# Kernel tuning notes

Measured on AMD Instinct MI355X. Metric: run time of the kernel, lower is better.

The kernel has to match this reference:

```python
import jax, jax.numpy as jnp
import numpy as np

N, F_IN, F_OUT = 8192, 512, 256


def setup_inputs() -> dict:
    key = jax.random.key(0)
    k1, k2, k3, k4 = jax.random.split(key, 4)
    x = jax.random.normal(k1, (N, F_IN), dtype=jnp.float32)
    adj = jax.random.randint(k2, (N, N), 0, 2, dtype=jnp.int32)
    # xavier_uniform with gain=1.414
    limW = 1.414 * np.sqrt(6.0 / (F_IN + F_OUT))
    W = jax.random.uniform(k3, (F_IN, F_OUT), dtype=jnp.float32, minval=-limW, maxval=limW)
    lima = 1.414 * np.sqrt(6.0 / (2 * F_OUT + 1))
    a = jax.random.uniform(k4, (2 * F_OUT, 1), dtype=jnp.float32, minval=-lima, maxval=lima)
    return {"x": x, "adj": adj, "W": W, "a": a}


def reference(x, adj, W, a):
    # h = x @ W : [N, F_out]
    h = x @ W
    f_out = h.shape[1]
    # additive score a^T [h_i ; h_j] is separable: (h @ a_l)_i + (h @ a_r)_j
    f_src = h @ a[:f_out, 0]   # [N]
    f_dst = h @ a[f_out:, 0]   # [N]
    e = jax.nn.leaky_relu(f_src[:, None] + f_dst[None, :], negative_slope=0.2)  # [N, N]
    e = jnp.where(adj > 0, e, jnp.float32(-9e15))
    attention = jax.nn.softmax(e, axis=1)  # row-wise over neighbors
    # dropout(p=0.6) is identity in eval mode
    h_prime = attention @ h  # [N, F_out]
    return h_prime
```

## Files before the change

kernel.cpp:

```cpp
#include <hip/hip_runtime.h>
#include <hip/hip_bf16.h>

#define NN 8192
#define FIN 512
#define FOUT 256
#define JTILE 64

typedef __attribute__((ext_vector_type(8))) short short8;
typedef __attribute__((ext_vector_type(4))) short short4v;
typedef __attribute__((ext_vector_type(4))) float float4v;
typedef __attribute__((ext_vector_type(16))) float float16v;

__device__ __forceinline__ short f2bf(float f) {
    union { float f; unsigned u; } v; v.f = f;
    unsigned r = (v.u + 0x7FFFu + ((v.u >> 16) & 1u)) >> 16;
    return (short)r;
}

__global__ __launch_bounds__(256) void wt_kernel(const float* __restrict__ W,
                                                 short* __restrict__ Wt) {
    __shared__ short tile[32][33];
    int tx = threadIdx.x & 31, ty = threadIdx.x >> 5;
    int k0 = blockIdx.x * 32, n0 = blockIdx.y * 32;
#pragma unroll
    for (int r = 0; r < 32; r += 8)
        tile[ty + r][tx] = f2bf(W[(size_t)(k0 + ty + r) * FOUT + n0 + tx]);
    __syncthreads();
#pragma unroll
    for (int r = 0; r < 32; r += 8)
        Wt[(size_t)(n0 + ty + r) * FIN + k0 + tx] = tile[tx][ty + r];
}

__global__ __launch_bounds__(256) void h_kernel(const float* __restrict__ x,
                                                const short* __restrict__ Wt,
                                                const float* __restrict__ a,
                                                short* __restrict__ h_t,
                                                float* __restrict__ f_src,
                                                float* __restrict__ f_dst) {
    int wave = (blockIdx.x << 2) + (threadIdx.x >> 6);
    int lane = threadIdx.x & 63;
    int m0 = (wave & 511) << 4;
    int n0 = (wave >> 9) << 6;
    int lr = lane & 15, lq = lane >> 4;

    const float* xrow = x + (size_t)(m0 + lr) * FIN + lq * 8;
    const short* wbase = Wt + (size_t)(n0 + lr) * FIN + lq * 8;

    float4v acc[4] = {};
    for (int k0 = 0; k0 < FIN; k0 += 32) {
        float4v xa = *(const float4v*)(xrow + k0);
        float4v xb = *(const float4v*)(xrow + k0 + 4);
        short8 av;
        av[0] = f2bf(xa[0]); av[1] = f2bf(xa[1]); av[2] = f2bf(xa[2]); av[3] = f2bf(xa[3]);
        av[4] = f2bf(xb[0]); av[5] = f2bf(xb[1]); av[6] = f2bf(xb[2]); av[7] = f2bf(xb[3]);
#pragma unroll
        for (int ct = 0; ct < 4; ct++) {
            short8 bv = *(const short8*)(wbase + (size_t)ct * 16 * FIN + k0);
            acc[ct] = __builtin_amdgcn_mfma_f32_16x16x32_bf16(av, bv, acc[ct], 0, 0, 0);
        }
    }
    float s_part[4] = {0.f, 0.f, 0.f, 0.f};
    float d_part[4] = {0.f, 0.f, 0.f, 0.f};
#pragma unroll
    for (int ct = 0; ct < 4; ct++) {
        int n = n0 + ct * 16 + lr;
        float al = a[n], ar = a[FOUT + n];
#pragma unroll
        for (int reg = 0; reg < 4; reg++) {
            float hv = acc[ct][reg];
            s_part[reg] = fmaf(hv, al, s_part[reg]);
            d_part[reg] = fmaf(hv, ar, d_part[reg]);
            h_t[(size_t)n * NN + (m0 + lq * 4 + reg)] = f2bf(hv);
        }
    }
#pragma unroll
    for (int off = 1; off < 16; off <<= 1) {
#pragma unroll
        for (int reg = 0; reg < 4; reg++) {
            s_part[reg] += __shfl_xor(s_part[reg], off);
            d_part[reg] += __shfl_xor(d_part[reg], off);
        }
    }
    const float LOG2E = 1.4426950408889634f;
    if (lr == 0) {
#pragma unroll
        for (int reg = 0; reg < 4; reg++) {
            atomicAdd(&f_src[m0 + lq * 4 + reg], s_part[reg] * LOG2E);
            atomicAdd(&f_dst[m0 + lq * 4 + reg], d_part[reg] * LOG2E);
        }
    }
}

__global__ __launch_bounds__(256, 2) void gat_kernel(const int* __restrict__ adj,
                                                     const short* __restrict__ h_t,
                                                     const float* __restrict__ f_src,
                                                     const float* __restrict__ f_dst,
                                                     float* __restrict__ Opart,
                                                     float* __restrict__ lpart,
                                                     int jlen) {
    __shared__ short Ht[256 * 72];
    __shared__ short Pt[64 * 72];
    __shared__ float Fd[2][64];

    const int t = threadIdx.x;
    const int i0 = blockIdx.x * 64;
    const int slice = blockIdx.y;
    const int jbase = slice * jlen;

    const int prow = t >> 2, pjq = t & 3;
    const int lane = t & 63, w = t >> 6;
    const int l31 = lane & 31, lq = lane >> 5;
    const int wn0 = w * 64;

    const float fs = f_src[i0 + prow];
    const int* adjRow = adj + (size_t)(i0 + prow) * NN;
    const short* hrow = h_t + ((size_t)t << 13);

    float16v acc00 = {}, acc01 = {}, acc10 = {}, acc11 = {};
    float lp = 0.f;

    if (t < 16) *(float4*)&Fd[0][t * 4] = *(const float4*)(f_dst + jbase + t * 4);
    int4 av0 = *(const int4*)(adjRow + jbase + pjq * 16);
    int4 av1 = *(const int4*)(adjRow + jbase + pjq * 16 + 4);
    int4 av2 = *(const int4*)(adjRow + jbase + pjq * 16 + 8);
    int4 av3 = *(const int4*)(adjRow + jbase + pjq * 16 + 12);
    __syncthreads();

    int buf = 0;
    for (int jo = 0; jo < jlen; jo += JTILE) {
        const int j0 = jbase + jo;
        {
            const float* fdc = &Fd[buf][pjq * 16];
            short8 pbl, pbh;
            int4 avs[4] = {av0, av1, av2, av3};
#pragma unroll
            for (int g = 0; g < 4; g++) {
                const int* ai = (const int*)&avs[g];
#pragma unroll
                for (int q = 0; q < 4; q++) {
                    float y = fs + fdc[g * 4 + q];
                    y = fmaxf(y, 0.2f * y);
                    float e = exp2f(y);
                    float p = (ai[q] != 0) ? e : 0.f;
                    lp += p;
                    short pb = f2bf(p);
                    if (g < 2) pbl[g * 4 + q] = pb; else pbh[(g - 2) * 4 + q] = pb;
                }
            }
            *(short8*)&Pt[prow * 72 + pjq * 16] = pbl;
            *(short8*)&Pt[prow * 72 + pjq * 16 + 8] = pbh;
        }
#pragma unroll
        for (int q = 0; q < 8; q++)
            *(short8*)&Ht[t * 72 + q * 8] = *(const short8*)(hrow + j0 + q * 8);

        if (jo + JTILE < jlen) {
            if (t < 16) *(float4*)&Fd[buf ^ 1][t * 4] = *(const float4*)(f_dst + j0 + JTILE + t * 4);
            av0 = *(const int4*)(adjRow + j0 + JTILE + pjq * 16);
            av1 = *(const int4*)(adjRow + j0 + JTILE + pjq * 16 + 4);
            av2 = *(const int4*)(adjRow + j0 + JTILE + pjq * 16 + 8);
            av3 = *(const int4*)(adjRow + j0 + JTILE + pjq * 16 + 12);
        }
        __syncthreads();

#pragma unroll
        for (int kk = 0; kk < 4; kk++) {
            short8 a0 = *(const short8*)&Pt[l31 * 72 + kk * 16 + lq * 8];
            short8 a1 = *(const short8*)&Pt[(32 + l31) * 72 + kk * 16 + lq * 8];
            short8 b0 = *(const short8*)&Ht[(wn0 + l31) * 72 + kk * 16 + lq * 8];
            short8 b1 = *(const short8*)&Ht[(wn0 + 32 + l31) * 72 + kk * 16 + lq * 8];
            acc00 = __builtin_amdgcn_mfma_f32_32x32x16_bf16(a0, b0, acc00, 0, 0, 0);
            acc01 = __builtin_amdgcn_mfma_f32_32x32x16_bf16(a0, b1, acc01, 0, 0, 0);
            acc10 = __builtin_amdgcn_mfma_f32_32x32x16_bf16(a1, b0, acc10, 0, 0, 0);
            acc11 = __builtin_amdgcn_mfma_f32_32x32x16_bf16(a1, b1, acc11, 0, 0, 0);
        }
        buf ^= 1;
        __syncthreads();
    }

    lp += __shfl_xor(lp, 1);
    lp += __shfl_xor(lp, 2);
    if (pjq == 0) lpart[slice * NN + i0 + prow] = lp;

    float* obase = Opart + ((size_t)slice * NN + i0) * FOUT;
#pragma unroll
    for (int rt = 0; rt < 2; rt++) {
#pragma unroll
        for (int nt = 0; nt < 2; nt++) {
            const float16v& av = rt == 0 ? (nt == 0 ? acc00 : acc01) : (nt == 0 ? acc10 : acc11);
#pragma unroll
            for (int reg = 0; reg < 16; reg++) {
                int row = rt * 32 + (reg & 3) + 8 * (reg >> 2) + 4 * lq;
                int n = wn0 + nt * 32 + l31;
                obase[(size_t)row * FOUT + n] = av[reg];
            }
        }
    }
}

__global__ __launch_bounds__(256) void combine_kernel(const float* __restrict__ Opart,
                                                      const float* __restrict__ lpart,
                                                      float* __restrict__ out, int slices) {
    int i = blockIdx.x, n = threadIdx.x;
    float o = 0.f, l = 0.f;
    for (int s = 0; s < slices; s++) {
        o += Opart[((size_t)s * NN + i) * FOUT + n];
        l += lpart[s * NN + i];
    }
    out[(size_t)i * FOUT + n] = o / l;
}

extern "C" void kernel_launch(void* const* d_in, const int* in_sizes, int n_in,
                              void* d_out, int out_size, void* d_ws, size_t ws_size,
                              hipStream_t stream) {
    const float* x   = (const float*)d_in[0];
    const int*   adj = (const int*)d_in[1];
    const float* W   = (const float*)d_in[2];
    const float* a   = (const float*)d_in[3];
    float* out = (float*)d_out;

    char* ws = (char*)d_ws;
    short* h_t   = (short*)ws;
    short* Wt    = (short*)(ws + (4u << 20));
    float* f_src = (float*)(ws + (4u << 20) + (256u << 10));
    float* f_dst = (float*)(ws + (4u << 20) + (288u << 10));
    float* lpart = (float*)(ws + (4u << 20) + (320u << 10));
    float* Opart = (float*)(ws + (5u << 20));

    const size_t OSLICE = (size_t)NN * FOUT * 4;
    int slices = 1;
    if (ws_size >= (5u << 20) + 4 * OSLICE) slices = 4;
    else if (ws_size >= (5u << 20) + 2 * OSLICE) slices = 2;
    int jlen = NN / slices;

    hipMemsetAsync(f_src, 0, 2 * NN * sizeof(float), stream);
    wt_kernel<<<dim3(FIN / 32, FOUT / 32), 256, 0, stream>>>(W, Wt);
    h_kernel<<<512, 256, 0, stream>>>(x, Wt, a, h_t, f_src, f_dst);
    gat_kernel<<<dim3(NN / 64, slices), 256, 0, stream>>>(adj, h_t, f_src, f_dst,
                                                          Opart, lpart, jlen);
    combine_kernel<<<NN, 256, 0, stream>>>(Opart, lpart, out, slices);
}
```

Measured before the change: 448.9 us.

## Load H tiles directly into registers, double-buffer swizzled P tile, single barrier

The GAT aggregation kernel no longer stages the h^T tile through shared memory. Each wave now loads its MFMA B operands straight from global memory into registers, which shrinks LDS use and allows raising launch bounds to 3 blocks per CU. The P tile is double-buffered with an XOR swizzle in place of padding, so each iteration needs only one barrier instead of two, and exp2 uses the hardware builtin. Up to 8 j-slices are allowed when workspace permits, which means more partial outputs for the combine kernel to read in exchange for more parallelism. The cost is redundant global loads of h across blocks and more register pressure.

```diff
diff --git a/kernel.cpp b/kernel.cpp
--- a/kernel.cpp
+++ b/kernel.cpp
@@ -7,9 +7,14 @@
 #define JTILE 64
 
 typedef __attribute__((ext_vector_type(8))) short short8;
-typedef __attribute__((ext_vector_type(4))) short short4v;
 typedef __attribute__((ext_vector_type(4))) float float4v;
 typedef __attribute__((ext_vector_type(16))) float float16v;
+
+#if __has_builtin(__builtin_amdgcn_exp2f)
+#define EXP2(x) __builtin_amdgcn_exp2f(x)
+#else
+#define EXP2(x) exp2f(x)
+#endif
 
 __device__ __forceinline__ short f2bf(float f) {
     union { float f; unsigned u; } v; v.f = f;
@@ -91,15 +96,14 @@
     }
 }
 
-__global__ __launch_bounds__(256, 2) void gat_kernel(const int* __restrict__ adj,
+__global__ __launch_bounds__(256, 3) void gat_kernel(const int* __restrict__ adj,
                                                      const short* __restrict__ h_t,
                                                      const float* __restrict__ f_src,
                                                      const float* __restrict__ f_dst,
                                                      float* __restrict__ Opart,
                                                      float* __restrict__ lpart,
                                                      int jlen) {
-    __shared__ short Ht[256 * 72];
-    __shared__ short Pt[64 * 72];
+    __shared__ short Pt[2][64 * 64];
     __shared__ float Fd[2][64];
 
     const int t = threadIdx.x;
@@ -113,69 +117,88 @@
     const int wn0 = w * 64;
 
     const float fs = f_src[i0 + prow];
-    const int* adjRow = adj + (size_t)(i0 + prow) * NN;
-    const short* hrow = h_t + ((size_t)t << 13);
+    const int* adjRow = adj + (size_t)(i0 + prow) * NN + jbase;
+    const short* hb0 = h_t + (size_t)(wn0 + l31) * NN + jbase + lq * 8;
+    const short* hb1 = hb0 + (size_t)32 * NN;
 
     float16v acc00 = {}, acc01 = {}, acc10 = {}, acc11 = {};
     float lp = 0.f;
 
     if (t < 16) *(float4*)&Fd[0][t * 4] = *(const float4*)(f_dst + jbase + t * 4);
-    int4 av0 = *(const int4*)(adjRow + jbase + pjq * 16);
-    int4 av1 = *(const int4*)(adjRow + jbase + pjq * 16 + 4);
-    int4 av2 = *(const int4*)(adjRow + jbase + pjq * 16 + 8);
-    int4 av3 = *(const int4*)(adjRow + jbase + pjq * 16 + 12);
+    int4 av0 = *(const int4*)(adjRow + pjq * 16);
+    int4 av1 = *(const int4*)(adjRow + pjq * 16 + 4);
+    int4 av2 = *(const int4*)(adjRow + pjq * 16 + 8);
+    int4 av3 = *(const int4*)(adjRow + pjq * 16 + 12);
     __syncthreads();
 
     int buf = 0;
+    const int pswz = (prow & 7) << 4;
+    const int rswz = (l31 & 7) << 4;
+    const int wb = prow * 128 + pjq * 32;
+
     for (int jo = 0; jo < jlen; jo += JTILE) {
-        const int j0 = jbase + jo;
+        short8 b0[4], b1[4];
+#pragma unroll
+        for (int kk = 0; kk < 4; kk++) {
+            b0[kk] = *(const short8*)(hb0 + jo + kk * 16);
+            b1[kk] = *(const short8*)(hb1 + jo + kk * 16);
+        }
+        const bool more = (jo + JTILE) < jlen;
+        const int* ap = adjRow + (more ? jo + JTILE : 0) + pjq * 16;
+        int4 an0 = *(const int4*)(ap);
+        int4 an1 = *(const int4*)(ap + 4);
+        int4 an2 = *(const int4*)(ap + 8);
+        int4 an3 = *(const int4*)(ap + 12);
+
         {
-            const float* fdc = &Fd[buf][pjq * 16];
+            const float4v fd0 = *(const float4v*)&Fd[buf][pjq * 16];
+            const float4v fd1 = *(const float4v*)&Fd[buf][pjq * 16 + 4];
+            const float4v fd2 = *(const float4v*)&Fd[buf][pjq * 16 + 8];
+            const float4v fd3 = *(const float4v*)&Fd[buf][pjq * 16 + 12];
             short8 pbl, pbh;
-            int4 avs[4] = {av0, av1, av2, av3};
-#pragma unroll
-            for (int g = 0; g < 4; g++) {
-                const int* ai = (const int*)&avs[g];
-#pragma unroll
-                for (int q = 0; q < 4; q++) {
-                    float y = fs + fdc[g * 4 + q];
-                    y = fmaxf(y, 0.2f * y);
-                    float e = exp2f(y);
-                    float p = (ai[q] != 0) ? e : 0.f;
-                    lp += p;
-                    short pb = f2bf(p);
-                    if (g < 2) pbl[g * 4 + q] = pb; else pbh[(g - 2) * 4 + q] = pb;
-                }
+#define PEL(A, FDV, DST, IDX)                              \
+            {                                              \
+                float y = fs + (FDV);                      \
+                y = fmaxf(y, 0.2f * y);                    \
+                float p = ((A) != 0) ? EXP2(y) : 0.f;      \
+                lp += p;                                   \
+                DST[IDX] = f2bf(p);                        \
             }
-            *(short8*)&Pt[prow * 72 + pjq * 16] = pbl;
-            *(short8*)&Pt[prow * 72 + pjq * 16 + 8] = pbh;
-        }
-#pragma unroll
-        for (int q = 0; q < 8; q++)
-            *(short8*)&Ht[t * 72 + q * 8] = *(const short8*)(hrow + j0 + q * 8);
-
-        if (jo + JTILE < jlen) {
-            if (t < 16) *(float4*)&Fd[buf ^ 1][t * 4] = *(const float4*)(f_dst + j0 + JTILE + t * 4);
-            av0 = *(const int4*)(adjRow + j0 + JTILE + pjq * 16);
-            av1 = *(const int4*)(adjRow + j0 + JTILE + pjq * 16 + 4);
-            av2 = *(const int4*)(adjRow + j0 + JTILE + pjq * 16 + 8);
-            av3 = *(const int4*)(adjRow + j0 + JTILE + pjq * 16 + 12);
-        }
-        __syncthreads();
-
-#pragma unroll
-        for (int kk = 0; kk < 4; kk++) {
-            short8 a0 = *(const short8*)&Pt[l31 * 72 + kk * 16 + lq * 8];
-            short8 a1 = *(const short8*)&Pt[(32 + l31) * 72 + kk * 16 + lq * 8];
-            short8 b0 = *(const short8*)&Ht[(wn0 + l31) * 72 + kk * 16 + lq * 8];
-            short8 b1 = *(const short8*)&Ht[(wn0 + 32 + l31) * 72 + kk * 16 + lq * 8];
-            acc00 = __builtin_amdgcn_mfma_f32_32x32x16_bf16(a0, b0, acc00, 0, 0, 0);
-            acc01 = __builtin_amdgcn_mfma_f32_32x32x16_bf16(a0, b1, acc01, 0, 0, 0);
-            acc10 = __builtin_amdgcn_mfma_f32_32x32x16_bf16(a1, b0, acc10, 0, 0, 0);
-            acc11 = __builtin_amdgcn_mfma_f32_32x32x16_bf16(a1, b1, acc11, 0, 0, 0);
-        }
+            PEL(av0.x, fd0[0], pbl, 0) PEL(av0.y, fd0[1], pbl, 1)
+            PEL(av0.z, fd0[2], pbl, 2) PEL(av0.w, fd0[3], pbl, 3)
+            PEL(av1.x, fd1[0], pbl, 4) PEL(av1.y, fd1[1], pbl, 5)
+            PEL(av1.z, fd1[2], pbl, 6) PEL(av1.w, fd1[3], pbl, 7)
+            PEL(av2.x, fd2[0], pbh, 0) PEL(av2.y, fd2[1], pbh, 1)
+            PEL(av2.z, fd2[2], pbh, 2) PEL(av2.w, fd2[3], pbh, 3)
+            PEL(av3.x, fd3[0], pbh, 4) PEL(av3.y, fd3[1], pbh, 5)
+            PEL(av3.z, fd3[2], pbh, 6) PEL(av3.w, fd3[3], pbh, 7)
+#undef PEL
+            char* pbuf = (char*)&Pt[buf][0];
+            *(short8*)(pbuf + (wb ^ pswz)) = pbl;
+            *(short8*)(pbuf + ((wb + 16) ^ pswz)) = pbh;
+        }
+        if (t < 16) {
+            float4 fdn = *(const float4*)(f_dst + jbase + (more ? jo + JTILE : 0) + t * 4);
+            *(float4*)&Fd[buf ^ 1][t * 4] = fdn;
+        }
+
+        asm volatile("s_waitcnt lgkmcnt(0)\n\ts_barrier" ::: "memory");
+
+        {
+            const char* pbuf = (const char*)&Pt[buf][0];
+            const int ra = l31 * 128 + lq * 16;
+#pragma unroll
+            for (int kk = 0; kk < 4; kk++) {
+                short8 a0 = *(const short8*)(pbuf + ((ra + kk * 32) ^ rswz));
+                short8 a1 = *(const short8*)(pbuf + ((ra + 4096 + kk * 32) ^ rswz));
+                acc00 = __builtin_amdgcn_mfma_f32_32x32x16_bf16(a0, b0[kk], acc00, 0, 0, 0);
+                acc01 = __builtin_amdgcn_mfma_f32_32x32x16_bf16(a0, b1[kk], acc01, 0, 0, 0);
+                acc10 = __builtin_amdgcn_mfma_f32_32x32x16_bf16(a1, b0[kk], acc10, 0, 0, 0);
+                acc11 = __builtin_amdgcn_mfma_f32_32x32x16_bf16(a1, b1[kk], acc11, 0, 0, 0);
+            }
+        }
+        av0 = an0; av1 = an1; av2 = an2; av3 = an3;
         buf ^= 1;
-        __syncthreads();
     }
 
     lp += __shfl_xor(lp, 1);
@@ -229,8 +252,9 @@
 
     const size_t OSLICE = (size_t)NN * FOUT * 4;
     int slices = 1;
-    if (ws_size >= (5u << 20) + 4 * OSLICE) slices = 4;
-    else if (ws_size >= (5u << 20) + 2 * OSLICE) slices = 2;
+    if (ws_size >= (size_t)(5u << 20) + 8 * OSLICE) slices = 8;
+    else if (ws_size >= (size_t)(5u << 20) + 4 * OSLICE) slices = 4;
+    else if (ws_size >= (size_t)(5u << 20) + 2 * OSLICE) slices = 2;
     int jlen = NN / slices;
 
     hipMemsetAsync(f_src, 0, 2 * NN * sizeof(float), stream);
```

Result: slower. 468.4 us (+4.3%).
